# Kernel optimization log

Hardware: AMD Instinct MI355X
Metric: run time of the kernel (lower is better)

Reference implementation:

```python
import jax, jax.numpy as jnp
import numpy as np

N_NODES = 200000
F_IN = 256
F_OUT = 256
N_GRAPHS = 512


def setup_inputs() -> dict:
    key = jax.random.key(0)
    k1, k2, k3 = jax.random.split(key, 3)
    x = jax.random.normal(k1, (N_NODES, F_IN), dtype=jnp.float32)
    batch = jnp.sort(jax.random.randint(k2, (N_NODES,), 0, N_GRAPHS, dtype=jnp.int32))
    kg, kn = jax.random.split(k3)
    # Linear weights, scaled like torch default init (~1/sqrt(fan_in))
    W_gate = jax.random.normal(kg, (F_IN, 1), dtype=jnp.float32) / np.sqrt(F_IN)
    b_gate = jnp.zeros((1,), dtype=jnp.float32)
    W_nn = jax.random.normal(kn, (F_IN, F_OUT), dtype=jnp.float32) / np.sqrt(F_IN)
    b_nn = jnp.zeros((F_OUT,), dtype=jnp.float32)
    return {"x": x, "batch": batch, "size": N_GRAPHS,
            "W_gate": W_gate, "b_gate": b_gate, "W_nn": W_nn, "b_nn": b_nn}


def reference(x, batch, size, W_gate, b_gate, W_nn, b_nn):
    # gate scores: h_gate(x) -> [N, 1]
    gate = x @ W_gate + b_gate
    # segment softmax over nodes of each graph (PyG-style, with 1e-16 eps)
    seg_max = jax.ops.segment_max(gate, batch, num_segments=size)   # [S, 1]
    gate = jnp.exp(gate - seg_max[batch])
    denom = jax.ops.segment_sum(gate, batch, num_segments=size)     # [S, 1]
    gate = gate / (denom[batch] + 1e-16)
    # h_theta(x) -> [N, F_OUT]
    h = x @ W_nn + b_nn
    # weighted scatter-add pooling -> [S, F_OUT]
    out = jax.ops.segment_sum(gate * h, batch, num_segments=size)
    return (out, gate)
```

## Files before the change

### kernel.cpp

```cpp
#include <hip/hip_runtime.h>
#include <math.h>

#define F        256
#define NGRAPH   512
#define BLOCK    1024
#define NWAVES   (BLOCK / 64)
#define GCAP     3072

typedef float f32x4 __attribute__((ext_vector_type(4)));

__global__ void gap_fused(const float* __restrict__ x,
                          const float* __restrict__ Wg,
                          const float* __restrict__ bg,
                          const float* __restrict__ Wnn,
                          const float* __restrict__ bnn,
                          const int* __restrict__ batch, int n_nodes,
                          float* __restrict__ out,
                          float* __restrict__ gate_out) {
    __shared__ int sbounds[2];
    __shared__ float glds[GCAP];
    __shared__ __align__(16) float wacc[NWAVES][F];
    __shared__ float wd[NWAVES];
    __shared__ float xbar[F];
    __shared__ float partial[BLOCK];

    const int s    = blockIdx.x;
    const int tid  = threadIdx.x;
    const int wid  = tid >> 6;
    const int lane = tid & 63;

    if (wid < 2) {
        const int v = s + wid;
        int lo = 0, hi = n_nodes;
        while (hi - lo > 64) {
            const int step = (hi - lo) >> 6;
            const int q    = lo + (lane + 1) * step;
            const bool c   = (q >= hi) ? true : (batch[q] >= v);
            const unsigned long long m = __ballot(c);
            if (m == 0ull) {
                lo = lo + (step << 6) + 1;
            } else {
                const int l0 = __ffsll((long long)m) - 1;
                const int qh = lo + (l0 + 1) * step;
                const int nlo = (l0 == 0) ? lo : (lo + l0 * step + 1);
                hi = qh < hi ? qh : hi;
                lo = nlo;
            }
        }
        const int q  = lo + lane;
        const bool c = (q < hi) && (batch[q] >= v);
        const unsigned long long m = __ballot(c);
        const int r = (m == 0ull) ? hi : (lo + __ffsll((long long)m) - 1);
        if (lane == 0) sbounds[wid] = r;
    }
    __syncthreads();
    const int lo  = sbounds[0];
    const int hi  = sbounds[1];
    const int cnt = hi - lo;

    const f32x4 wg  = reinterpret_cast<const f32x4*>(Wg)[lane];
    const float bgv = bg[0];

    float d = 0.f;
    float ax = 0.f, ay = 0.f, az = 0.f, aw = 0.f;

    int n = lo + (wid << 2);
    for (; n + 3 < hi; n += 4 * NWAVES) {
        const f32x4* rp = reinterpret_cast<const f32x4*>(x + (size_t)n * F) + lane;
        const f32x4 x0 = __builtin_nontemporal_load(rp);
        const f32x4 x1 = __builtin_nontemporal_load(rp + 64);
        const f32x4 x2 = __builtin_nontemporal_load(rp + 128);
        const f32x4 x3 = __builtin_nontemporal_load(rp + 192);

        float p0 = x0.x * wg.x + x0.y * wg.y + x0.z * wg.z + x0.w * wg.w;
        float p1 = x1.x * wg.x + x1.y * wg.y + x1.z * wg.z + x1.w * wg.w;
        float p2 = x2.x * wg.x + x2.y * wg.y + x2.z * wg.z + x2.w * wg.w;
        float p3 = x3.x * wg.x + x3.y * wg.y + x3.z * wg.z + x3.w * wg.w;
        #pragma unroll
        for (int o = 32; o > 0; o >>= 1) {
            p0 += __shfl_xor(p0, o);
            p1 += __shfl_xor(p1, o);
            p2 += __shfl_xor(p2, o);
            p3 += __shfl_xor(p3, o);
        }
        const float e0 = __expf(p0 + bgv);
        const float e1 = __expf(p1 + bgv);
        const float e2 = __expf(p2 + bgv);
        const float e3 = __expf(p3 + bgv);

        const int idx = n - lo;
        if (lane == 0 && idx + 3 < GCAP) {
            glds[idx]     = e0;
            glds[idx + 1] = e1;
            glds[idx + 2] = e2;
            glds[idx + 3] = e3;
        }
        d += (e0 + e1) + (e2 + e3);
        ax += e0 * x0.x + e1 * x1.x + e2 * x2.x + e3 * x3.x;
        ay += e0 * x0.y + e1 * x1.y + e2 * x2.y + e3 * x3.y;
        az += e0 * x0.z + e1 * x1.z + e2 * x2.z + e3 * x3.z;
        aw += e0 * x0.w + e1 * x1.w + e2 * x2.w + e3 * x3.w;
    }
    for (int t = n; t < hi && t < n + 4; ++t) {
        const f32x4 xv = *(reinterpret_cast<const f32x4*>(x + (size_t)t * F) + lane);
        float p = xv.x * wg.x + xv.y * wg.y + xv.z * wg.z + xv.w * wg.w;
        #pragma unroll
        for (int o = 32; o > 0; o >>= 1) p += __shfl_xor(p, o);
        const float e = __expf(p + bgv);
        if (lane == 0 && (t - lo) < GCAP) glds[t - lo] = e;
        d += e;
        ax += e * xv.x; ay += e * xv.y; az += e * xv.z; aw += e * xv.w;
    }

    if (lane == 0) wd[wid] = d;
    f32x4 av; av.x = ax; av.y = ay; av.z = az; av.w = aw;
    reinterpret_cast<f32x4*>(&wacc[wid][0])[lane] = av;
    __syncthreads();

    if (cnt > 0) {
        float D = 0.f;
        #pragma unroll
        for (int w = 0; w < NWAVES; ++w) D += wd[w];
        const float inv = 1.f / (D + 1e-16f);

        if (tid < F) {
            float v = 0.f;
            #pragma unroll
            for (int w = 0; w < NWAVES; ++w) v += wacc[w][tid];
            xbar[tid] = v * inv;
        }

        const int nl = cnt < GCAP ? cnt : GCAP;
        for (int idx = tid; idx < nl; idx += BLOCK) {
            gate_out[lo + idx] = glds[idx] * inv;
        }
        for (int t = lo + GCAP + wid; t < hi; t += NWAVES) {
            const f32x4 xv = *(reinterpret_cast<const f32x4*>(x + (size_t)t * F) + lane);
            float p = xv.x * wg.x + xv.y * wg.y + xv.z * wg.z + xv.w * wg.w;
            #pragma unroll
            for (int o = 32; o > 0; o >>= 1) p += __shfl_xor(p, o);
            if (lane == 0) gate_out[t] = __expf(p + bgv) * inv;
        }
        __syncthreads();

        const int q  = tid >> 8;
        const int j  = tid & 255;
        const int k0 = q * 64;
        float sum = 0.f;
        #pragma unroll 8
        for (int k = k0; k < k0 + 64; ++k) sum += xbar[k] * Wnn[k * F + j];
        partial[tid] = sum;
        __syncthreads();
        if (tid < F) {
            out[(size_t)s * F + tid] = partial[tid] + partial[F + tid] +
                                       partial[2 * F + tid] + partial[3 * F + tid] + bnn[tid];
        }
    } else {
        if (tid < F) out[(size_t)s * F + tid] = 0.f;
    }
}

extern "C" void kernel_launch(void* const* d_in, const int* in_sizes, int n_in,
                              void* d_out, int out_size, void* d_ws, size_t ws_size,
                              hipStream_t stream) {
    const float* x     = (const float*)d_in[0];
    const int*   batch = (const int*)d_in[1];
    const float* Wg    = (const float*)d_in[3];
    const float* bg    = (const float*)d_in[4];
    const float* Wnn   = (const float*)d_in[5];
    const float* bnn   = (const float*)d_in[6];

    float* out  = (float*)d_out;
    float* gate = out + (size_t)NGRAPH * F;

    const int N = in_sizes[0] / F;

    gap_fused<<<NGRAPH, BLOCK, 0, stream>>>(x, Wg, bg, Wnn, bnn, batch, N, out, gate);
}
```

Before: 42.68 us.

## Split each wave into four 16-lane groups, one node row per group

Remaps the main streaming loop so each wave handles four rows at once, with each 16-lane group owning one row and each lane loading four float4 chunks. This cuts the per-row gate dot-product reduction from six shuffle steps to four and removes the scalar tail loop by predicating inactive rows. The cost is a cross-group shuffle reduction of 17 accumulators at the end and a different per-lane memory access pattern.

```diff
diff --git a/kernel.cpp b/kernel.cpp
--- a/kernel.cpp
+++ b/kernel.cpp
@@ -8,6 +8,10 @@
 #define GCAP     3072
 
 typedef float f32x4 __attribute__((ext_vector_type(4)));
+
+__device__ __forceinline__ float dot4(f32x4 a, f32x4 b) {
+    return a.x * b.x + a.y * b.y + a.z * b.z + a.w * b.w;
+}
 
 __global__ void gap_fused(const float* __restrict__ x,
                           const float* __restrict__ Wg,
@@ -58,63 +62,66 @@
     const int hi  = sbounds[1];
     const int cnt = hi - lo;
 
-    const f32x4 wg  = reinterpret_cast<const f32x4*>(Wg)[lane];
+    const int j   = lane & 15;
+    const int grp = lane >> 4;
+
+    const f32x4* wgp = reinterpret_cast<const f32x4*>(Wg);
+    const f32x4 wg0 = wgp[j];
+    const f32x4 wg1 = wgp[j + 16];
+    const f32x4 wg2 = wgp[j + 32];
+    const f32x4 wg3 = wgp[j + 48];
     const float bgv = bg[0];
 
     float d = 0.f;
-    float ax = 0.f, ay = 0.f, az = 0.f, aw = 0.f;
+    f32x4 a0 = {0.f, 0.f, 0.f, 0.f}, a1 = a0, a2 = a0, a3 = a0;
 
-    int n = lo + (wid << 2);
-    for (; n + 3 < hi; n += 4 * NWAVES) {
-        const f32x4* rp = reinterpret_cast<const f32x4*>(x + (size_t)n * F) + lane;
-        const f32x4 x0 = __builtin_nontemporal_load(rp);
-        const f32x4 x1 = __builtin_nontemporal_load(rp + 64);
-        const f32x4 x2 = __builtin_nontemporal_load(rp + 128);
-        const f32x4 x3 = __builtin_nontemporal_load(rp + 192);
+    for (int n = lo + (wid << 2); n < hi; n += 4 * NWAVES) {
+        const int r    = n + grp;
+        const bool act = (r < hi);
+        const int rc   = act ? r : (hi - 1);
+        const f32x4* rp = reinterpret_cast<const f32x4*>(x + (size_t)rc * F);
+        const f32x4 x0 = __builtin_nontemporal_load(rp + j);
+        const f32x4 x1 = __builtin_nontemporal_load(rp + j + 16);
+        const f32x4 x2 = __builtin_nontemporal_load(rp + j + 32);
+        const f32x4 x3 = __builtin_nontemporal_load(rp + j + 48);
 
-        float p0 = x0.x * wg.x + x0.y * wg.y + x0.z * wg.z + x0.w * wg.w;
-        float p1 = x1.x * wg.x + x1.y * wg.y + x1.z * wg.z + x1.w * wg.w;
-        float p2 = x2.x * wg.x + x2.y * wg.y + x2.z * wg.z + x2.w * wg.w;
-        float p3 = x3.x * wg.x + x3.y * wg.y + x3.z * wg.z + x3.w * wg.w;
-        #pragma unroll
-        for (int o = 32; o > 0; o >>= 1) {
-            p0 += __shfl_xor(p0, o);
-            p1 += __shfl_xor(p1, o);
-            p2 += __shfl_xor(p2, o);
-            p3 += __shfl_xor(p3, o);
-        }
-        const float e0 = __expf(p0 + bgv);
-        const float e1 = __expf(p1 + bgv);
-        const float e2 = __expf(p2 + bgv);
-        const float e3 = __expf(p3 + bgv);
+        float p = dot4(x0, wg0) + dot4(x1, wg1) + dot4(x2, wg2) + dot4(x3, wg3);
+        p += __shfl_xor(p, 1);
+        p += __shfl_xor(p, 2);
+        p += __shfl_xor(p, 4);
+        p += __shfl_xor(p, 8);
 
-        const int idx = n - lo;
-        if (lane == 0 && idx + 3 < GCAP) {
-            glds[idx]     = e0;
-            glds[idx + 1] = e1;
-            glds[idx + 2] = e2;
-            glds[idx + 3] = e3;
-        }
-        d += (e0 + e1) + (e2 + e3);
-        ax += e0 * x0.x + e1 * x1.x + e2 * x2.x + e3 * x3.x;
-        ay += e0 * x0.y + e1 * x1.y + e2 * x2.y + e3 * x3.y;
-        az += e0 * x0.z + e1 * x1.z + e2 * x2.z + e3 * x3.z;
-        aw += e0 * x0.w + e1 * x1.w + e2 * x2.w + e3 * x3.w;
-    }
-    for (int t = n; t < hi && t < n + 4; ++t) {
-        const f32x4 xv = *(reinterpret_cast<const f32x4*>(x + (size_t)t * F) + lane);
-        float p = xv.x * wg.x + xv.y * wg.y + xv.z * wg.z + xv.w * wg.w;
-        #pragma unroll
-        for (int o = 32; o > 0; o >>= 1) p += __shfl_xor(p, o);
-        const float e = __expf(p + bgv);
-        if (lane == 0 && (t - lo) < GCAP) glds[t - lo] = e;
+        const float e = act ? __expf(p + bgv) : 0.f;
+        const int idx = r - lo;
+        if (j == 0 && act && idx < GCAP) glds[idx] = e;
+
         d += e;
-        ax += e * xv.x; ay += e * xv.y; az += e * xv.z; aw += e * xv.w;
+        a0 += e * x0;
+        a1 += e * x1;
+        a2 += e * x2;
+        a3 += e * x3;
     }
 
+    #pragma unroll
+    for (int o = 16; o <= 32; o <<= 1) {
+        d += __shfl_xor(d, o);
+        a0.x += __shfl_xor(a0.x, o); a0.y += __shfl_xor(a0.y, o);
+        a0.z += __shfl_xor(a0.z, o); a0.w += __shfl_xor(a0.w, o);
+        a1.x += __shfl_xor(a1.x, o); a1.y += __shfl_xor(a1.y, o);
+        a1.z += __shfl_xor(a1.z, o); a1.w += __shfl_xor(a1.w, o);
+        a2.x += __shfl_xor(a2.x, o); a2.y += __shfl_xor(a2.y, o);
+        a2.z += __shfl_xor(a2.z, o); a2.w += __shfl_xor(a2.w, o);
+        a3.x += __shfl_xor(a3.x, o); a3.y += __shfl_xor(a3.y, o);
+        a3.z += __shfl_xor(a3.z, o); a3.w += __shfl_xor(a3.w, o);
+    }
     if (lane == 0) wd[wid] = d;
-    f32x4 av; av.x = ax; av.y = ay; av.z = az; av.w = aw;
-    reinterpret_cast<f32x4*>(&wacc[wid][0])[lane] = av;
+    if (grp == 0) {
+        f32x4* wp = reinterpret_cast<f32x4*>(&wacc[wid][0]);
+        wp[j]      = a0;
+        wp[j + 16] = a1;
+        wp[j + 32] = a2;
+        wp[j + 48] = a3;
+    }
     __syncthreads();
 
     if (cnt > 0) {
@@ -134,21 +141,24 @@
         for (int idx = tid; idx < nl; idx += BLOCK) {
             gate_out[lo + idx] = glds[idx] * inv;
         }
-        for (int t = lo + GCAP + wid; t < hi; t += NWAVES) {
-            const f32x4 xv = *(reinterpret_cast<const f32x4*>(x + (size_t)t * F) + lane);
-            float p = xv.x * wg.x + xv.y * wg.y + xv.z * wg.z + xv.w * wg.w;
-            #pragma unroll
-            for (int o = 32; o > 0; o >>= 1) p += __shfl_xor(p, o);
-            if (lane == 0) gate_out[t] = __expf(p + bgv) * inv;
+        for (int t = lo + GCAP + (tid >> 4); t < hi; t += BLOCK / 16) {
+            const f32x4* rp = reinterpret_cast<const f32x4*>(x + (size_t)t * F);
+            float p = dot4(rp[j], wg0) + dot4(rp[j + 16], wg1) +
+                      dot4(rp[j + 32], wg2) + dot4(rp[j + 48], wg3);
+            p += __shfl_xor(p, 1);
+            p += __shfl_xor(p, 2);
+            p += __shfl_xor(p, 4);
+            p += __shfl_xor(p, 8);
+            if (j == 0) gate_out[t] = __expf(p + bgv) * inv;
         }
         __syncthreads();
 
         const int q  = tid >> 8;
-        const int j  = tid & 255;
+        const int jj = tid & 255;
         const int k0 = q * 64;
         float sum = 0.f;
         #pragma unroll 8
-        for (int k = k0; k < k0 + 64; ++k) sum += xbar[k] * Wnn[k * F + j];
+        for (int k = k0; k < k0 + 64; ++k) sum += xbar[k] * Wnn[k * F + jj];
         partial[tid] = sum;
         __syncthreads();
         if (tid < F) {
```

Result: slower. 44.41 us (+4.1%).
